# Kernel tuning notes

Hardware: AMD Instinct MI355X
Metric: run time of the kernel (lower is better)

Reference implementation:

```python
import jax, jax.numpy as jnp
import numpy as np

B, S, D = 8, 1025, 768
H, KV, HD = 12, 4, 64
GH, GW = 32, 32
EPS = 1e-6


def setup_inputs() -> dict:
    key = jax.random.key(0)
    ks = jax.random.split(key, 6)
    sc = 0.02
    hidden_states = jax.random.normal(ks[0], (B, S, D), jnp.float32)
    attention_mask = jnp.ones((B, S), dtype=bool)
    image_pos_ids = jnp.broadcast_to(jnp.arange(S, dtype=jnp.int32), (B, S))
    return dict(
        hidden_states=hidden_states,
        attention_mask=attention_mask,
        image_pos_ids=image_pos_ids,
        grid_h=GH,
        grid_w=GW,
        Wq=jax.random.normal(ks[1], (D, H * HD), jnp.float32) * sc,
        Wk=jax.random.normal(ks[2], (D, KV * HD), jnp.float32) * sc,
        Wv=jax.random.normal(ks[3], (D, KV * HD), jnp.float32) * sc,
        Wo=jax.random.normal(ks[4], (H * HD, D), jnp.float32) * sc,
        q_norm_w=jnp.ones((HD,), jnp.float32),
        k_norm_w=jnp.ones((HD,), jnp.float32),
    )


def _rmsnorm(x, w, eps=EPS):
    return x * jax.lax.rsqrt(jnp.mean(x * x, axis=-1, keepdims=True) + eps) * w


def _rotate(x, cos, sin):
    # x: [B, h, P, HD]; cos/sin: [B, P, HD//2]. Pairs are adjacent (view_as_complex).
    hd = x.shape[-1]
    xr = x.reshape(*x.shape[:-1], hd // 2, 2)
    x0, x1 = xr[..., 0], xr[..., 1]
    c, s = cos[:, None], sin[:, None]  # broadcast over heads
    o0 = x0 * c - x1 * s
    o1 = x0 * s + x1 * c
    return jnp.stack([o0, o1], axis=-1).reshape(x.shape)


def reference(hidden_states, attention_mask, image_pos_ids, grid_h, grid_w,
              Wq, Wk, Wv, Wo, q_norm_w, k_norm_w):
    b, s, d = hidden_states.shape
    hd = q_norm_w.shape[0]
    h = Wq.shape[1] // hd
    kv = Wk.shape[1] // hd
    n_rep = h // kv
    scale = hd ** -0.5

    q = _rmsnorm((hidden_states @ Wq).reshape(b, s, h, hd), q_norm_w).transpose(0, 2, 1, 3)
    k = _rmsnorm((hidden_states @ Wk).reshape(b, s, kv, hd), k_norm_w).transpose(0, 2, 1, 3)
    v = (hidden_states @ Wv).reshape(b, s, kv, hd).transpose(0, 2, 1, 3)

    # 2D RoPE on patch tokens only (CLS token at position 0 excluded)
    ids = image_pos_ids[:, 1:]
    hi = (ids // grid_w) % grid_h
    wi = ids % grid_w
    half, quarter = hd // 2, hd // 4
    inv_freq = 1.0 / (10000.0 ** (jnp.arange(quarter, dtype=jnp.float32) * 2.0 / half))
    ang = jnp.concatenate([hi[..., None] * inv_freq, wi[..., None] * inv_freq], axis=-1)  # [B,P,HD/2]
    cos, sin = jnp.cos(ang), jnp.sin(ang)
    q = jnp.concatenate([q[:, :, :1], _rotate(q[:, :, 1:], cos, sin)], axis=2)
    k = jnp.concatenate([k[:, :, :1], _rotate(k[:, :, 1:], cos, sin)], axis=2)

    # GQA: repeat_interleave kv heads to match query heads
    kr = jnp.repeat(k, n_rep, axis=1)
    vr = jnp.repeat(v, n_rep, axis=1)

    scores = jnp.einsum('bhqd,bhkd->bhqk', q, kr) * scale
    add = jnp.where(attention_mask, 0.0, jnp.finfo(jnp.float32).min)[:, None, None, :]
    scores = scores + add
    attn = jax.nn.softmax(scores.astype(jnp.float32), axis=-1).astype(q.dtype)
    out = jnp.einsum('bhqk,bhkd->bqhd', attn, vr).reshape(b, s, h * hd)
    return (out @ Wo, attn)
```

## Files before the change

kernel.cpp:

```cpp
#include <hip/hip_runtime.h>
#include <hip/hip_fp16.h>

#define B_ 8
#define S_ 1025
#define D_ 768
#define H_ 12
#define KV_ 4
#define HD_ 64
#define NREP 3
#define SCALE_ 0.125f
#define EPS_ 1e-6f
#define SKP 1088
#define HSS 1092
#define QBLK 16
#define NQT 65
#define DYNLDS 34944

#define PROW(r) ((r) * HSS + 4 * ((r) & 1))

typedef __attribute__((ext_vector_type(8))) short bf16x8;
typedef __attribute__((ext_vector_type(4))) float f32x4;

__device__ __forceinline__ unsigned short f2bf(float f) {
  unsigned int u = __builtin_bit_cast(unsigned int, f);
  return (unsigned short)((u + 0x7FFFu + ((u >> 16) & 1u)) >> 16);
}
__device__ __forceinline__ unsigned int pk2(float a, float b) {
  return (unsigned int)f2bf(a) | ((unsigned int)f2bf(b) << 16);
}
__device__ __forceinline__ float bf2f(unsigned short u) {
  return __builtin_bit_cast(float, (unsigned int)u << 16);
}

__device__ __forceinline__ void barrier_lgkm() {
  __builtin_amdgcn_sched_barrier(0);
  asm volatile("s_waitcnt lgkmcnt(0)" ::: "memory");
  __builtin_amdgcn_s_barrier();
  __builtin_amdgcn_sched_barrier(0);
}

__global__ __launch_bounds__(256) void cast_x_kernel(const float* __restrict__ x,
                                                     unsigned short* __restrict__ xb, int n4) {
  int i = blockIdx.x * 256 + threadIdx.x;
  if (i >= n4) return;
  f32x4 v = *(const f32x4*)(x + (size_t)i * 4);
  uint2 o;
  o.x = pk2(v[0], v[1]);
  o.y = pk2(v[2], v[3]);
  *(uint2*)(xb + (size_t)i * 4) = o;
}

__global__ __launch_bounds__(256) void cast_wqkv_kernel(const float* __restrict__ Wq,
    const float* __restrict__ Wk, const float* __restrict__ Wv,
    unsigned short* __restrict__ WT) {
  int idx = blockIdx.x * 256 + threadIdx.x;
  int n = idx / D_, k = idx % D_;
  float v;
  if (n < 768)       v = Wq[(size_t)k * 768 + n];
  else if (n < 1024) v = Wk[(size_t)k * 256 + (n - 768)];
  else               v = Wv[(size_t)k * 256 + (n - 1024)];
  WT[idx] = f2bf(v);
}

__global__ __launch_bounds__(256) void cast_wo_kernel(const float* __restrict__ Wo,
                                                      unsigned short* __restrict__ WT) {
  int idx = blockIdx.x * 256 + threadIdx.x;
  int n = idx / D_, k = idx % D_;
  WT[idx] = f2bf(Wo[(size_t)k * D_ + n]);
}

#define BM 128
#define BN 128
#define BK 32
#define LSTR 40
__global__ __launch_bounds__(256) void gemm_bt(const unsigned short* __restrict__ A,
    const unsigned short* __restrict__ BT, float* __restrict__ C, int M, int N, int K) {
  __shared__ unsigned short As[BM * LSTR];
  __shared__ unsigned short Bs[BN * LSTR];
  const int nMt = (M + BM - 1) / BM;
  const int tm = blockIdx.x % nMt;
  const int tn = blockIdx.x / nMt;
  const int row0 = tm * BM, col0 = tn * BN;
  const int tid = threadIdx.x;
  const int l = tid & 63, w = tid >> 6;
  const int wr = (w >> 1) * 64, wc = (w & 1) * 64;
  const int lr = l & 15, lk = (l >> 4) * 8;
  f32x4 acc[4][4] = {};
  for (int kt = 0; kt < K; kt += BK) {
    __syncthreads();
#pragma unroll
    for (int i = 0; i < 2; ++i) {
      int c = tid + i * 256;
      int r = c >> 2;
      int ce = (c & 3) * 8;
      int gr = row0 + r; gr = gr < M ? gr : M - 1;
      bf16x8 va = *(const bf16x8*)(A + (size_t)gr * K + kt + ce);
      *(bf16x8*)&As[r * LSTR + ce] = va;
      bf16x8 vb = *(const bf16x8*)(BT + (size_t)(col0 + r) * K + kt + ce);
      *(bf16x8*)&Bs[r * LSTR + ce] = vb;
    }
    __syncthreads();
    bf16x8 af[4], bfr[4];
#pragma unroll
    for (int m = 0; m < 4; ++m)
      af[m] = *(const bf16x8*)&As[(wr + m * 16 + lr) * LSTR + lk];
#pragma unroll
    for (int n = 0; n < 4; ++n)
      bfr[n] = *(const bf16x8*)&Bs[(wc + n * 16 + lr) * LSTR + lk];
#pragma unroll
    for (int m = 0; m < 4; ++m)
#pragma unroll
      for (int n = 0; n < 4; ++n)
        acc[m][n] = __builtin_amdgcn_mfma_f32_16x16x32_bf16(af[m], bfr[n], acc[m][n], 0, 0, 0);
  }
  const int orow = (l >> 4) * 4;
#pragma unroll
  for (int m = 0; m < 4; ++m)
#pragma unroll
    for (int n = 0; n < 4; ++n)
#pragma unroll
      for (int r = 0; r < 4; ++r) {
        int row = row0 + wr + m * 16 + orow + r;
        int col = col0 + wc + n * 16 + lr;
        if (row < M) C[(size_t)row * N + col] = acc[m][n][r];
      }
}

__global__ __launch_bounds__(256) void qkv_epilogue(const float* __restrict__ QKV,
    const int* __restrict__ pos_ids, const int* __restrict__ ghp, const int* __restrict__ gwp,
    const float* __restrict__ qw, const float* __restrict__ kw,
    unsigned short* __restrict__ Qb, unsigned short* __restrict__ Kb,
    unsigned short* __restrict__ Vt) {
  if (blockIdx.x < B_ * KV_) {
    unsigned short* vp = Vt + (size_t)blockIdx.x * 64 * SKP;
    for (int idx = threadIdx.x; idx < 64 * 63; idx += 256) {
      int d = idx / 63, s = S_ + idx % 63;
      vp[d * SKP + s] = 0;
    }
  }
  int tok = blockIdx.x * 4 + (threadIdx.x >> 6);
  int l = threadIdx.x & 63;
  if (tok >= B_ * S_) return;
  int b = tok / S_, s = tok % S_;
  const float* rowp = QKV + (size_t)tok * 1280;
  bool rot = (s > 0);
  float cs = 1.f, sn = 0.f;
  if (rot) {
    int gh = ghp[0], gw = gwp[0];
    int pos = pos_ids[tok];
    int hi = (pos / gw) % gh;
    int wi = pos % gw;
    int pi = l >> 1;
    int j = pi < 16 ? pi : pi - 16;
    float invf = exp2f(-(float)j * (13.287712379549449f / 16.f));
    float ang = (pi < 16 ? (float)hi : (float)wi) * invf;
    cs = cosf(ang); sn = sinf(ang);
  }
#pragma unroll
  for (int h = 0; h < H_; ++h) {
    float x = rowp[h * 64 + l];
    float ss = x * x;
    for (int off = 32; off; off >>= 1) ss += __shfl_xor(ss, off);
    float xn = x * rsqrtf(ss * (1.f / 64.f) + EPS_) * qw[l];
    float o = xn;
    if (rot) {
      float p = __shfl_xor(xn, 1);
      o = (l & 1) ? (p * sn + xn * cs) : (xn * cs - p * sn);
    }
    o *= SCALE_;
    Qb[((size_t)(b * H_ + h) * S_ + s) * 64 + l] = f2bf(o);
  }
#pragma unroll
  for (int h = 0; h < KV_; ++h) {
    float x = rowp[768 + h * 64 + l];
    float ss = x * x;
    for (int off = 32; off; off >>= 1) ss += __shfl_xor(ss, off);
    float xn = x * rsqrtf(ss * (1.f / 64.f) + EPS_) * kw[l];
    float o = xn;
    if (rot) {
      float p = __shfl_xor(xn, 1);
      o = (l & 1) ? (p * sn + xn * cs) : (xn * cs - p * sn);
    }
    Kb[((size_t)(b * KV_ + h) * S_ + s) * 64 + l] = f2bf(o);
    float v = rowp[1024 + h * 64 + l];
    Vt[((size_t)(b * KV_ + h) * 64 + l) * SKP + s] = f2bf(v);
  }
}

__global__ __launch_bounds__(512, 8) void attn_kernel(const unsigned short* __restrict__ Qb,
    const unsigned short* __restrict__ Kb, const unsigned short* __restrict__ Vt,
    unsigned short* __restrict__ ctx, float* __restrict__ attn_out) {
  extern __shared__ unsigned short Ush[];
  __shared__ float partial[4][64][4];
  int bid = blockIdx.x;
  int swz = (bid & 7) * 780 + (bid >> 3);
  int qt = swz % NQT;
  int h = (swz / NQT) % H_;
  int b = swz / (NQT * H_);
  int kvh = h / NREP;
  int q0 = qt * QBLK;
  int tid = threadIdx.x;
  int l = tid & 63, w = tid >> 6;
  int lr = l & 15, lk = (l >> 4) * 8;

  const unsigned short* Qbase = Qb + (size_t)(b * H_ + h) * S_ * 64;
  const unsigned short* Kbase = Kb + (size_t)(b * KV_ + kvh) * S_ * 64;
  const unsigned short* Vbase = Vt + (size_t)(b * KV_ + kvh) * 64 * SKP;

  int qrow = q0 + lr; if (qrow >= S_) qrow = S_ - 1;
  bf16x8 qf0 = *(const bf16x8*)(Qbase + (size_t)qrow * 64 + lk);
  bf16x8 qf1 = *(const bf16x8*)(Qbase + (size_t)qrow * 64 + 32 + lk);

  {
    const int kcol = w * 16 + lr;
    const int nT = (w < 4) ? 9 : 8;
    const unsigned short* kp = Kbase + (size_t)kcol * 64;
    bf16x8 kf0 = *(const bf16x8*)(kp + lk);
    bf16x8 kf1 = *(const bf16x8*)(kp + 32 + lk);
    for (int t = 0; t < nT; ++t) {
      bf16x8 nf0 = kf0, nf1 = kf1;
      if (t + 1 < nT) {
        int kr = (t + 1) * 128 + kcol; if (kr >= S_) kr = S_ - 1;
        const unsigned short* np = Kbase + (size_t)kr * 64;
        nf0 = *(const bf16x8*)(np + lk);
        nf1 = *(const bf16x8*)(np + 32 + lk);
      }
      f32x4 acc = {};
      acc = __builtin_amdgcn_mfma_f32_16x16x32_bf16(qf0, kf0, acc, 0, 0, 0);
      acc = __builtin_amdgcn_mfma_f32_16x16x32_bf16(qf1, kf1, acc, 0, 0, 0);
      int col = t * 128 + kcol;
      int rowb = (l >> 4) * 4;
#pragma unroll
      for (int r = 0; r < 4; ++r)
        Ush[(size_t)(rowb + r) * HSS + col] =
            __builtin_bit_cast(unsigned short, __float2half(acc[r]));
      kf0 = nf0; kf1 = nf1;
    }
  }
  barrier_lgkm();

#pragma unroll
  for (int rr = 0; rr < 2; ++rr) {
    int rowi = w + rr * 8;
    const unsigned short* Hrow = Ush + (size_t)rowi * HSS;
    float f[17];
    float mx = -1e30f;
#pragma unroll
    for (int i = 0; i < 17; ++i) {
      int key = l + i * 64;
      float v = (key < S_) ? __half2float(__builtin_bit_cast(__half, Hrow[key])) : -1e30f;
      f[i] = v;
      mx = fmaxf(mx, v);
    }
    for (int off = 32; off; off >>= 1) mx = fmaxf(mx, __shfl_xor(mx, off));
    float sum = 0.f;
#pragma unroll
    for (int i = 0; i < 17; ++i) {
      float e = __expf(f[i] - mx);
      f[i] = e; sum += e;
    }
    for (int off = 32; off; off >>= 1) sum += __shfl_xor(sum, off);
    float inv = 1.f / sum;
    unsigned short* Prow = Ush + PROW(rowi);
#pragma unroll
    for (int i = 0; i < 17; ++i) {
      int key = l + i * 64;
      Prow[key] = f2bf((key < S_) ? f[i] * inv : 0.f);
    }
  }

#pragma unroll
  for (int rr = 0; rr < 2; ++rr) {
    int rowi = w + rr * 8;
    int q = q0 + rowi;
    if (q < S_) {
      const unsigned short* Prow = Ush + PROW(rowi);
      float* gout = attn_out + ((size_t)(b * H_ + h) * S_ + q) * S_;
      int a = (4 - (q & 3)) & 3;
      int rem = 1025 - a;
      int nx4 = rem >> 2, tail = rem & 3;
      if (l < a) gout[l] = bf2f(Prow[l]);
      if (l < tail) { int idx = a + 4 * nx4 + l; gout[idx] = bf2f(Prow[idx]); }
#pragma unroll
      for (int c = 0; c < 4; ++c) {
        int j = c * 64 + l;
        if (j < nx4) {
          int d0 = a + 4 * j;
          f32x4 o;
          o[0] = bf2f(Prow[d0]);
          o[1] = bf2f(Prow[d0 + 1]);
          o[2] = bf2f(Prow[d0 + 2]);
          o[3] = bf2f(Prow[d0 + 3]);
          *(f32x4*)(gout + d0) = o;
        }
      }
    }
  }
  barrier_lgkm();

  f32x4 accv = {};
  {
    const int d0 = (w & 3) * 16;
    const int kh = (w >> 2) * 544;
    const int prow = PROW(lr);
    const unsigned short* vb = Vbase + (size_t)(d0 + lr) * SKP + kh;
#pragma unroll 4
    for (int kc = 0; kc < 17; ++kc) {
      bf16x8 pa = *(const bf16x8*)&Ush[prow + kh + kc * 32 + lk];
      bf16x8 vf = *(const bf16x8*)(vb + kc * 32 + lk);
      accv = __builtin_amdgcn_mfma_f32_16x16x32_bf16(pa, vf, accv, 0, 0, 0);
    }
  }
  if (w >= 4) *(f32x4*)partial[w - 4][l] = accv;
  barrier_lgkm();
  unsigned short* ctxs = Ush;
  if (w < 4) {
    accv += *(const f32x4*)partial[w][l];
    int rowb = (l >> 4) * 4;
    int d0 = (w & 3) * 16;
#pragma unroll
    for (int r = 0; r < 4; ++r)
      ctxs[(rowb + r) * 64 + d0 + lr] = f2bf(accv[r]);
  }
  barrier_lgkm();
  {
    int t = 2 * w + (l >> 5);
    int q = q0 + t;
    if (q < S_) {
      unsigned int u = *(const unsigned int*)&ctxs[t * 64 + 2 * (l & 31)];
      *(unsigned int*)(ctx + (size_t)(b * S_ + q) * 768 + h * 64 + 2 * (l & 31)) = u;
    }
  }
}

extern "C" void kernel_launch(void* const* d_in, const int* in_sizes, int n_in,
                              void* d_out, int out_size, void* d_ws, size_t ws_size,
                              hipStream_t stream) {
  const float* hidden = (const float*)d_in[0];
  const int* pos_ids = (const int*)d_in[2];
  const int* ghp = (const int*)d_in[3];
  const int* gwp = (const int*)d_in[4];
  const float* Wq = (const float*)d_in[5];
  const float* Wk = (const float*)d_in[6];
  const float* Wv = (const float*)d_in[7];
  const float* Wo = (const float*)d_in[8];
  const float* qnw = (const float*)d_in[9];
  const float* knw = (const float*)d_in[10];

  char* ws = (char*)d_ws;
  unsigned short* Xb    = (unsigned short*)ws;
  unsigned short* WqkvT = (unsigned short*)(ws + 12595200);
  unsigned short* WoT   = (unsigned short*)(ws + 14561280);
  float*          QKV   = (float*)(ws + 15740928);
  unsigned short* ctx   = (unsigned short*)(ws + 15740928);
  unsigned short* Qb    = (unsigned short*)(ws + 57724928);
  unsigned short* Kb    = (unsigned short*)(ws + 70320128);
  unsigned short* Vt    = (unsigned short*)(ws + 74518528);

  float* out0 = (float*)d_out;
  float* attn_out = out0 + (size_t)B_ * S_ * D_;

  cast_x_kernel<<<6150, 256, 0, stream>>>(hidden, Xb, 1574400);
  cast_wqkv_kernel<<<3840, 256, 0, stream>>>(Wq, Wk, Wv, WqkvT);
  cast_wo_kernel<<<2304, 256, 0, stream>>>(Wo, WoT);

  gemm_bt<<<65 * 10, 256, 0, stream>>>(Xb, WqkvT, QKV, B_ * S_, 1280, D_);

  qkv_epilogue<<<2050, 256, 0, stream>>>(QKV, pos_ids, ghp, gwp, qnw, knw, Qb, Kb, Vt);

  hipFuncSetAttribute((const void*)attn_kernel,
                      hipFuncAttributeMaxDynamicSharedMemorySize, DYNLDS);
  attn_kernel<<<B_ * H_ * NQT, 512, DYNLDS, stream>>>(Qb, Kb, Vt, ctx, attn_out);

  gemm_bt<<<65 * 6, 256, 0, stream>>>(ctx, WoT, out0, B_ * S_, D_, D_);
}
```

Baseline: 340.4 us.

## Fuse exp into QK^T, defer softmax normalization, vectorize attention-prob stores

The attention kernel now applies exp directly to the QK^T MFMA outputs and drops the separate max-reduction softmax pass. Row sums are accumulated in registers and reduced through a small shared array. Normalization is deferred: it is applied to the PV output and to the probabilities when they are written out. The attention-probability store now runs after the context write, using aligned packed LDS reads specialised per row alignment, and launch bounds drop to 4 waves per EU. Skipping the max subtraction relies on scores staying small because Q and K are RMS-normalised, so large norm weights could overflow exp.

```diff
diff --git a/kernel.cpp b/kernel.cpp
--- a/kernel.cpp
+++ b/kernel.cpp
@@ -1,5 +1,4 @@
 #include <hip/hip_runtime.h>
-#include <hip/hip_fp16.h>
 
 #define B_ 8
 #define S_ 1025
@@ -11,12 +10,10 @@
 #define SCALE_ 0.125f
 #define EPS_ 1e-6f
 #define SKP 1088
-#define HSS 1092
+#define PST 1096
 #define QBLK 16
 #define NQT 65
-#define DYNLDS 34944
-
-#define PROW(r) ((r) * HSS + 4 * ((r) & 1))
+#define DYNLDS 35072
 
 typedef __attribute__((ext_vector_type(8))) short bf16x8;
 typedef __attribute__((ext_vector_type(4))) float f32x4;
@@ -30,6 +27,11 @@
 }
 __device__ __forceinline__ float bf2f(unsigned short u) {
   return __builtin_bit_cast(float, (unsigned int)u << 16);
+}
+__device__ __forceinline__ unsigned int cvtpk(float a, float b) {
+  unsigned int r;
+  asm("v_cvt_pk_bf16_f32 %0, %1, %2" : "=v"(r) : "v"(a), "v"(b));
+  return r;
 }
 
 __device__ __forceinline__ void barrier_lgkm() {
@@ -187,11 +189,13 @@
   }
 }
 
-__global__ __launch_bounds__(512, 8) void attn_kernel(const unsigned short* __restrict__ Qb,
+__global__ __launch_bounds__(512, 4) void attn_kernel(const unsigned short* __restrict__ Qb,
     const unsigned short* __restrict__ Kb, const unsigned short* __restrict__ Vt,
     unsigned short* __restrict__ ctx, float* __restrict__ attn_out) {
-  extern __shared__ unsigned short Ush[];
+  extern __shared__ unsigned short Psh[];
   __shared__ float partial[4][64][4];
+  __shared__ float red[8][16];
+  __shared__ unsigned short ctxs[16][64];
   int bid = blockIdx.x;
   int swz = (bid & 7) * 780 + (bid >> 3);
   int qt = swz % NQT;
@@ -211,124 +215,156 @@
   bf16x8 qf0 = *(const bf16x8*)(Qbase + (size_t)qrow * 64 + lk);
   bf16x8 qf1 = *(const bf16x8*)(Qbase + (size_t)qrow * 64 + 32 + lk);
 
+  float psum = 0.f;
   {
-    const int kcol = w * 16 + lr;
-    const int nT = (w < 4) ? 9 : 8;
-    const unsigned short* kp = Kbase + (size_t)kcol * 64;
-    bf16x8 kf0 = *(const bf16x8*)(kp + lk);
-    bf16x8 kf1 = *(const bf16x8*)(kp + 32 + lk);
-    for (int t = 0; t < nT; ++t) {
-      bf16x8 nf0 = kf0, nf1 = kf1;
-      if (t + 1 < nT) {
-        int kr = (t + 1) * 128 + kcol; if (kr >= S_) kr = S_ - 1;
-        const unsigned short* np = Kbase + (size_t)kr * 64;
-        nf0 = *(const bf16x8*)(np + lk);
-        nf1 = *(const bf16x8*)(np + 32 + lk);
+    const int g4 = (l >> 4) * 4;
+    const int kb = (w < 4) ? w * 144 : 576 + (w - 4) * 128;
+#pragma unroll
+    for (int j = 0; j < 9; ++j) {
+      if (w < 4 || j < 8) {
+        int kr = kb + j * 16 + lr; if (kr > 1024) kr = 1024;
+        const unsigned short* kp = Kbase + (size_t)kr * 64;
+        bf16x8 kf0 = *(const bf16x8*)(kp + lk);
+        bf16x8 kf1 = *(const bf16x8*)(kp + 32 + lk);
+        f32x4 acc = {};
+        acc = __builtin_amdgcn_mfma_f32_16x16x32_bf16(kf0, qf0, acc, 0, 0, 0);
+        acc = __builtin_amdgcn_mfma_f32_16x16x32_bf16(kf1, qf1, acc, 0, 0, 0);
+        int key0 = kb + j * 16 + g4;
+        float e0 = (key0     <= 1024) ? __expf(acc[0]) : 0.f;
+        float e1 = (key0 + 1 <= 1024) ? __expf(acc[1]) : 0.f;
+        float e2 = (key0 + 2 <= 1024) ? __expf(acc[2]) : 0.f;
+        float e3 = (key0 + 3 <= 1024) ? __expf(acc[3]) : 0.f;
+        psum += (e0 + e1) + (e2 + e3);
+        uint2 pw; pw.x = cvtpk(e0, e1); pw.y = cvtpk(e2, e3);
+        *(uint2*)&Psh[(size_t)lr * PST + key0] = pw;
       }
-      f32x4 acc = {};
-      acc = __builtin_amdgcn_mfma_f32_16x16x32_bf16(qf0, kf0, acc, 0, 0, 0);
-      acc = __builtin_amdgcn_mfma_f32_16x16x32_bf16(qf1, kf1, acc, 0, 0, 0);
-      int col = t * 128 + kcol;
-      int rowb = (l >> 4) * 4;
-#pragma unroll
-      for (int r = 0; r < 4; ++r)
-        Ush[(size_t)(rowb + r) * HSS + col] =
-            __builtin_bit_cast(unsigned short, __float2half(acc[r]));
-      kf0 = nf0; kf1 = nf1;
-    }
-  }
+    }
+  }
+  psum += __shfl_xor(psum, 16);
+  psum += __shfl_xor(psum, 32);
+  if (l < 16) red[w][l] = psum;
   barrier_lgkm();
 
-#pragma unroll
-  for (int rr = 0; rr < 2; ++rr) {
-    int rowi = w + rr * 8;
-    const unsigned short* Hrow = Ush + (size_t)rowi * HSS;
-    float f[17];
-    float mx = -1e30f;
-#pragma unroll
-    for (int i = 0; i < 17; ++i) {
-      int key = l + i * 64;
-      float v = (key < S_) ? __half2float(__builtin_bit_cast(__half, Hrow[key])) : -1e30f;
-      f[i] = v;
-      mx = fmaxf(mx, v);
-    }
-    for (int off = 32; off; off >>= 1) mx = fmaxf(mx, __shfl_xor(mx, off));
-    float sum = 0.f;
-#pragma unroll
-    for (int i = 0; i < 17; ++i) {
-      float e = __expf(f[i] - mx);
-      f[i] = e; sum += e;
-    }
-    for (int off = 32; off; off >>= 1) sum += __shfl_xor(sum, off);
-    float inv = 1.f / sum;
-    unsigned short* Prow = Ush + PROW(rowi);
-#pragma unroll
-    for (int i = 0; i < 17; ++i) {
-      int key = l + i * 64;
-      Prow[key] = f2bf((key < S_) ? f[i] * inv : 0.f);
-    }
-  }
-
-#pragma unroll
-  for (int rr = 0; rr < 2; ++rr) {
-    int rowi = w + rr * 8;
-    int q = q0 + rowi;
-    if (q < S_) {
-      const unsigned short* Prow = Ush + PROW(rowi);
-      float* gout = attn_out + ((size_t)(b * H_ + h) * S_ + q) * S_;
-      int a = (4 - (q & 3)) & 3;
-      int rem = 1025 - a;
-      int nx4 = rem >> 2, tail = rem & 3;
-      if (l < a) gout[l] = bf2f(Prow[l]);
-      if (l < tail) { int idx = a + 4 * nx4 + l; gout[idx] = bf2f(Prow[idx]); }
-#pragma unroll
-      for (int c = 0; c < 4; ++c) {
-        int j = c * 64 + l;
-        if (j < nx4) {
-          int d0 = a + 4 * j;
-          f32x4 o;
-          o[0] = bf2f(Prow[d0]);
-          o[1] = bf2f(Prow[d0 + 1]);
-          o[2] = bf2f(Prow[d0 + 2]);
-          o[3] = bf2f(Prow[d0 + 3]);
-          *(f32x4*)(gout + d0) = o;
-        }
-      }
-    }
-  }
-  barrier_lgkm();
+  float invq;
+  {
+    float s = 0.f;
+#pragma unroll
+    for (int j2 = 0; j2 < 8; ++j2) s += red[j2][lr];
+    invq = 1.f / s;
+  }
 
   f32x4 accv = {};
   {
     const int d0 = (w & 3) * 16;
     const int kh = (w >> 2) * 544;
-    const int prow = PROW(lr);
+    const int prow = lr * PST + kh;
     const unsigned short* vb = Vbase + (size_t)(d0 + lr) * SKP + kh;
 #pragma unroll 4
     for (int kc = 0; kc < 17; ++kc) {
-      bf16x8 pa = *(const bf16x8*)&Ush[prow + kh + kc * 32 + lk];
+      bf16x8 pa = *(const bf16x8*)&Psh[prow + kc * 32 + lk];
       bf16x8 vf = *(const bf16x8*)(vb + kc * 32 + lk);
       accv = __builtin_amdgcn_mfma_f32_16x16x32_bf16(pa, vf, accv, 0, 0, 0);
     }
   }
   if (w >= 4) *(f32x4*)partial[w - 4][l] = accv;
   barrier_lgkm();
-  unsigned short* ctxs = Ush;
   if (w < 4) {
     accv += *(const f32x4*)partial[w][l];
     int rowb = (l >> 4) * 4;
     int d0 = (w & 3) * 16;
 #pragma unroll
-    for (int r = 0; r < 4; ++r)
-      ctxs[(rowb + r) * 64 + d0 + lr] = f2bf(accv[r]);
+    for (int r = 0; r < 4; ++r) {
+      float iv = __shfl(invq, rowb + r);
+      ctxs[rowb + r][d0 + lr] = f2bf(accv[r] * iv);
+    }
   }
   barrier_lgkm();
   {
     int t = 2 * w + (l >> 5);
     int q = q0 + t;
     if (q < S_) {
-      unsigned int u = *(const unsigned int*)&ctxs[t * 64 + 2 * (l & 31)];
+      unsigned int u = *(const unsigned int*)&ctxs[t][2 * (l & 31)];
       *(unsigned int*)(ctx + (size_t)(b * S_ + q) * 768 + h * 64 + 2 * (l & 31)) = u;
+    }
+  }
+
+#pragma unroll
+  for (int rr = 0; rr < 2; ++rr) {
+    int rowi = w + rr * 8;
+    int q = q0 + rowi;
+    if (q < S_) {
+      float rinv = __shfl(invq, rowi);
+      const unsigned short* Prow = Psh + (size_t)rowi * PST;
+      float* gout = attn_out + ((size_t)(b * H_ + h) * S_ + q) * S_;
+      int a = (4 - (q & 3)) & 3;
+      int nx4 = (1025 - a) >> 2;
+      int tl = 1025 - a - 4 * nx4;
+      if (l < a) gout[l] = bf2f(Prow[l]) * rinv;
+      if (l < tl) { int idx = a + 4 * nx4 + l; gout[idx] = bf2f(Prow[idx]) * rinv; }
+      if (a == 0) {
+#pragma unroll
+        for (int c = 0; c < 4; ++c) {
+          int ch = c * 64 + l;
+          if (ch < nx4) {
+            uint2 u = *(const uint2*)&Prow[4 * ch];
+            f32x4 o;
+            o[0] = __builtin_bit_cast(float, u.x << 16) * rinv;
+            o[1] = __builtin_bit_cast(float, u.x & 0xffff0000u) * rinv;
+            o[2] = __builtin_bit_cast(float, u.y << 16) * rinv;
+            o[3] = __builtin_bit_cast(float, u.y & 0xffff0000u) * rinv;
+            *(f32x4*)(gout + 4 * ch) = o;
+          }
+        }
+      } else if (a == 2) {
+#pragma unroll
+        for (int c = 0; c < 4; ++c) {
+          int ch = c * 64 + l;
+          if (ch < nx4) {
+            unsigned int u0 = *(const unsigned int*)&Prow[4 * ch + 2];
+            unsigned int u1 = *(const unsigned int*)&Prow[4 * ch + 4];
+            f32x4 o;
+            o[0] = __builtin_bit_cast(float, u0 << 16) * rinv;
+            o[1] = __builtin_bit_cast(float, u0 & 0xffff0000u) * rinv;
+            o[2] = __builtin_bit_cast(float, u1 << 16) * rinv;
+            o[3] = __builtin_bit_cast(float, u1 & 0xffff0000u) * rinv;
+            *(f32x4*)(gout + 2 + 4 * ch) = o;
+          }
+        }
+      } else if (a == 1) {
+#pragma unroll
+        for (int c = 0; c < 4; ++c) {
+          int ch = c * 64 + l;
+          if (ch < nx4) {
+            uint2 d01 = *(const uint2*)&Prow[4 * ch];
+            unsigned int d2 = *(const unsigned int*)&Prow[4 * ch + 4];
+            unsigned int u0 = __builtin_amdgcn_alignbit(d01.y, d01.x, 16);
+            unsigned int u1 = __builtin_amdgcn_alignbit(d2, d01.y, 16);
+            f32x4 o;
+            o[0] = __builtin_bit_cast(float, u0 << 16) * rinv;
+            o[1] = __builtin_bit_cast(float, u0 & 0xffff0000u) * rinv;
+            o[2] = __builtin_bit_cast(float, u1 << 16) * rinv;
+            o[3] = __builtin_bit_cast(float, u1 & 0xffff0000u) * rinv;
+            *(f32x4*)(gout + 1 + 4 * ch) = o;
+          }
+        }
+      } else {
+#pragma unroll
+        for (int c = 0; c < 4; ++c) {
+          int ch = c * 64 + l;
+          if (ch < nx4) {
+            unsigned int d0 = *(const unsigned int*)&Prow[4 * ch + 2];
+            uint2 d12 = *(const uint2*)&Prow[4 * ch + 4];
+            unsigned int u0 = __builtin_amdgcn_alignbit(d12.x, d0, 16);
+            unsigned int u1 = __builtin_amdgcn_alignbit(d12.y, d12.x, 16);
+            f32x4 o;
+            o[0] = __builtin_bit_cast(float, u0 << 16) * rinv;
+            o[1] = __builtin_bit_cast(float, u0 & 0xffff0000u) * rinv;
+            o[2] = __builtin_bit_cast(float, u1 << 16) * rinv;
+            o[3] = __builtin_bit_cast(float, u1 & 0xffff0000u) * rinv;
+            *(f32x4*)(gout + 3 + 4 * ch) = o;
+          }
+        }
+      }
     }
   }
 }
```

Result: no change. 340.3 us (-0.1%).
